# Optimization experiments

Hardware: AMD Instinct MI355X
Metric: run time of the kernel (lower is better)

Reference implementation:

```python
import jax, jax.numpy as jnp
import numpy as np
import math

NH = 12      # num attention heads
WIN = 128    # one-sided sliding window
NG = 32      # number of global (prefix) tokens
NEG = -1e9
LN_EPS = 1e-12


def _layernorm(x, g, b):
    mu = jnp.mean(x, axis=-1, keepdims=True)
    var = jnp.mean(jnp.square(x - mu), axis=-1, keepdims=True)
    return (x - mu) * jax.lax.rsqrt(var + LN_EPS) * g + b


def _longformer_self_attn(h, am, Wq, bq, Wk, bk, Wv, bv):
    B, S, D = h.shape
    Dh = D // NH
    w = WIN
    C = S // w  # number of chunks

    def proj(Wm, bm):
        return (h @ Wm + bm).reshape(B, S, NH, Dh).transpose(0, 2, 1, 3)

    q = proj(Wq, bq) * (1.0 / math.sqrt(Dh))  # [B,H,S,Dh]
    k = proj(Wk, bk)
    v = proj(Wv, bv)

    # ---- banded (sliding window) scores, chunked: each query chunk sees 3w keys ----
    kp = jnp.pad(k, ((0, 0), (0, 0), (w, w), (0, 0)))
    vp = jnp.pad(v, ((0, 0), (0, 0), (w, w), (0, 0)))
    idx = jnp.arange(C)[:, None] * w + jnp.arange(3 * w)[None, :]  # [C,3w]
    k3 = kp[:, :, idx]  # [B,H,C,3w,Dh]
    v3 = vp[:, :, idx]
    qc = q.reshape(B, NH, C, w, Dh)
    band = jnp.einsum('bhcqd,bhckd->bhcqk', qc, k3)  # [B,H,C,w,3w]

    qpos = (jnp.arange(C) * w)[:, None, None] + jnp.arange(w)[None, :, None]  # [C,w,1]
    kpos = (idx - w)[:, None, :]  # [C,1,3w] absolute key positions
    valid = (jnp.abs(kpos - qpos) <= w) & (kpos >= NG) & (kpos < S)  # band, exclude global keys

    amp = jnp.pad(am, ((0, 0), (w, w)))
    am3 = amp[:, idx]  # [B,C,3w] additive mask gathered per chunk
    band = band + am3[:, None, :, None, :]
    band = jnp.where(valid[None, None], band, NEG)
    band = band.reshape(B, NH, S, 3 * w)

    # ---- every token also attends to the NG global tokens ----
    gsc = jnp.einsum('bhsd,bhgd->bhsg', q, k[:, :, :NG]) + am[:, None, None, :NG]

    logits = jnp.concatenate([band, gsc], axis=-1)  # [B,H,S,3w+NG]
    probs = jax.nn.softmax(logits, axis=-1)
    pb = probs[..., :3 * w].reshape(B, NH, C, w, 3 * w)
    out = jnp.einsum('bhcqk,bhckd->bhcqd', pb, v3).reshape(B, NH, S, Dh)
    out = out + jnp.einsum('bhsg,bhgd->bhsd', probs[..., 3 * w:], v[:, :, :NG])

    # ---- global tokens attend to everything ----
    gl = jnp.einsum('bhgd,bhsd->bhgs', q[:, :, :NG], k) + am[:, None, None, :]
    outg = jnp.einsum('bhgs,bhsd->bhgd', jax.nn.softmax(gl, axis=-1), v)

    ctx = jnp.concatenate([outg, out[:, :, NG:]], axis=2)  # [B,H,S,Dh]
    return ctx.transpose(0, 2, 1, 3).reshape(B, S, D)


def setup_inputs() -> dict:
    key = jax.random.key(0)
    ks = jax.random.split(key, 8)
    B, S, D, F = 2, 4096, 768, 3072
    p = lambda k_, sh: jax.random.normal(k_, sh, jnp.float32) * 0.02
    return {
        'hidden_states': jax.random.normal(ks[0], (B, S, D), jnp.float32),
        'attention_mask': jnp.zeros((B, S), jnp.float32),
        'Wq': p(ks[1], (D, D)), 'bq': jnp.zeros((D,), jnp.float32),
        'Wk': p(ks[2], (D, D)), 'bk': jnp.zeros((D,), jnp.float32),
        'Wv': p(ks[3], (D, D)), 'bv': jnp.zeros((D,), jnp.float32),
        'Wo': p(ks[4], (D, D)), 'bo': jnp.zeros((D,), jnp.float32),
        'ln1_g': jnp.ones((D,), jnp.float32), 'ln1_b': jnp.zeros((D,), jnp.float32),
        'Wi': p(ks[5], (D, F)), 'bi': jnp.zeros((F,), jnp.float32),
        'Wo2': p(ks[6], (F, D)), 'bo2': jnp.zeros((D,), jnp.float32),
        'ln2_g': jnp.ones((D,), jnp.float32), 'ln2_b': jnp.zeros((D,), jnp.float32),
    }


def reference(hidden_states, attention_mask, Wq, bq, Wk, bk, Wv, bv, Wo, bo,
              ln1_g, ln1_b, Wi, bi, Wo2, bo2, ln2_g, ln2_b):
    ctx = _longformer_self_attn(hidden_states, attention_mask, Wq, bq, Wk, bk, Wv, bv)
    attn_out = _layernorm(ctx @ Wo + bo + hidden_states, ln1_g, ln1_b)
    inter = jax.nn.gelu(attn_out @ Wi + bi, approximate=False)
    layer_out = _layernorm(inter @ Wo2 + bo2 + attn_out, ln2_g, ln2_b)
    return layer_out
```

## Files before the change

### kernel.cpp

```cpp
#include <hip/hip_runtime.h>
#include <math.h>

#define NHEAD 12
#define DH 64
#define S_LEN 4096
#define B_SZ 2
#define D_MODEL 768
#define FF_DIM 3072
#define WINSZ 128
#define NGLB 32
#define NEGV -1e9f
#define NQC 6291456L

typedef __attribute__((ext_vector_type(8))) short bf16x8;
typedef __attribute__((ext_vector_type(4))) float floatx4;

__device__ __forceinline__ unsigned short f2bf(float x) {
    union { float f; unsigned u; } v; v.f = x;
    unsigned r = v.u + 0x7fffu + ((v.u >> 16) & 1u);
    return (unsigned short)(r >> 16);
}
__device__ __forceinline__ float bf2f(unsigned short x) {
    union { unsigned u; float f; } v; v.u = ((unsigned)x) << 16;
    return v.f;
}

__device__ __forceinline__ void async_copy16(const unsigned short* g, unsigned short* l) {
    __builtin_amdgcn_global_load_lds(
        (const __attribute__((address_space(1))) void*)g,
        (__attribute__((address_space(3))) void*)l, 16, 0, 0);
}

__global__ __launch_bounds__(256) void prep_k(
    const float* __restrict__ Wq, const float* __restrict__ Wk,
    const float* __restrict__ Wv, const float* __restrict__ Wo,
    const float* __restrict__ Wi, const float* __restrict__ Wo2,
    unsigned short* __restrict__ wqt, unsigned short* __restrict__ wkt,
    unsigned short* __restrict__ wvt, unsigned short* __restrict__ wot,
    unsigned short* __restrict__ wit, unsigned short* __restrict__ wo2t,
    const float* __restrict__ bq, const float* __restrict__ bk,
    const float* __restrict__ bv, float* __restrict__ bcat,
    const float* __restrict__ hid, unsigned short* __restrict__ hidb)
{
    __shared__ float tile[32][33];
    const int bid = blockIdx.x;
    const int tx = threadIdx.x, ty = threadIdx.y;

    if (bid < 6912) {
        const float* src; unsigned short* dst; int K, N, nx, local; float scale = 1.f;
        if (bid < 576)       { src = Wq;  dst = wqt;  K = 768;  N = 768;  nx = 24; local = bid;        scale = 0.125f; }
        else if (bid < 1152) { src = Wk;  dst = wkt;  K = 768;  N = 768;  nx = 24; local = bid - 576;  }
        else if (bid < 1728) { src = Wv;  dst = wvt;  K = 768;  N = 768;  nx = 24; local = bid - 1152; }
        else if (bid < 2304) { src = Wo;  dst = wot;  K = 768;  N = 768;  nx = 24; local = bid - 1728; }
        else if (bid < 4608) { src = Wi;  dst = wit;  K = 768;  N = 3072; nx = 96; local = bid - 2304; }
        else                 { src = Wo2; dst = wo2t; K = 3072; N = 768;  nx = 24; local = bid - 4608; }
        const int n0 = (local % nx) * 32, k0 = (local / nx) * 32;
#pragma unroll
        for (int i = 0; i < 4; ++i)
            tile[ty + 8 * i][tx] = src[(long)(k0 + ty + 8 * i) * N + n0 + tx];
        __syncthreads();
#pragma unroll
        for (int i = 0; i < 4; ++i)
            dst[(long)(n0 + ty + 8 * i) * K + k0 + tx] = f2bf(tile[tx][ty + 8 * i] * scale);
    } else if (bid < 6921) {
        const int t = ty * 32 + tx;
        const int i = (bid - 6912) * 256 + t;
        if (i < 768) bcat[i] = bq[i] * 0.125f;
        else if (i < 1536) bcat[i] = bk[i - 768];
        else if (i < 2304) bcat[i] = bv[i - 1536];
    } else {
        const int t = ty * 32 + tx;
        const long i = ((long)(bid - 6921) * 256 + t) * 4;
        float4 v = *(const float4*)(hid + i);
        ushort4 o;
        o.x = f2bf(v.x); o.y = f2bf(v.y); o.z = f2bf(v.z); o.w = f2bf(v.w);
        *(ushort4*)(hidb + i) = o;
    }
}

__global__ __launch_bounds__(256) void vt_k(
    const unsigned short* __restrict__ v, unsigned short* __restrict__ vt)
{
    const int bh = blockIdx.y;
    const int s0 = blockIdx.x * 32;
    const int w = threadIdx.x >> 6, lane = threadIdx.x & 63;
    const unsigned short* src = v + ((long)bh * S_LEN + s0 + w * 8) * DH + lane;
    unsigned short r[8];
#pragma unroll
    for (int j = 0; j < 8; ++j) r[j] = src[j * DH];
    unsigned short* dst = vt + ((long)bh * DH + lane) * S_LEN + s0 + w * 8;
    ushort4 lo, hi;
    lo.x = r[0]; lo.y = r[1]; lo.z = r[2]; lo.w = r[3];
    hi.x = r[4]; hi.y = r[5]; hi.z = r[6]; hi.w = r[7];
    *(ushort4*)dst = lo;
    *(ushort4*)(dst + 4) = hi;
}

template <int EPI>
__global__ __launch_bounds__(256) void gemm_bf(
    const unsigned short* __restrict__ A, const unsigned short* __restrict__ BT,
    const float* __restrict__ bias, void* __restrict__ out,
    int M, int N, int K, int nx)
{
    __shared__ unsigned short As[128 * 32];
    __shared__ unsigned short Bs[128 * 32];
    const int tid = threadIdx.x;
    const int wave = tid >> 6, lane = tid & 63;
    const int t8 = (blockIdx.x & 7) * (gridDim.x >> 3) + (blockIdx.x >> 3);
    const int m0 = (t8 / nx) * 128, n0 = (t8 % nx) * 128;
    const int wr = (wave >> 1) * 64, wc = (wave & 1) * 64;

    floatx4 acc[4][4];
#pragma unroll
    for (int i = 0; i < 4; ++i)
#pragma unroll
        for (int j = 0; j < 4; ++j) acc[i][j] = (floatx4){0.f, 0.f, 0.f, 0.f};

    const int srow = lane >> 2;
    const int schk = (((lane & 3) ^ (srow & 3))) * 8;
    const int r = lane & 15;
    const int q8 = ((lane >> 4) ^ (lane & 3)) * 8;

    for (int k0 = 0; k0 < K; k0 += 32) {
#pragma unroll
        for (int gi = 0; gi < 2; ++gi) {
            const int g = wave * 2 + gi;
            async_copy16(A + (long)(m0 + g * 16 + srow) * K + k0 + schk, &As[g * 512]);
            async_copy16(BT + (long)(n0 + g * 16 + srow) * K + k0 + schk, &Bs[g * 512]);
        }
        __syncthreads();

        bf16x8 af[4], bfr[4];
#pragma unroll
        for (int i = 0; i < 4; ++i) {
            af[i]  = *(const bf16x8*)&As[(wr + i * 16 + r) * 32 + q8];
            bfr[i] = *(const bf16x8*)&Bs[(wc + i * 16 + r) * 32 + q8];
        }
#pragma unroll
        for (int i = 0; i < 4; ++i)
#pragma unroll
            for (int j = 0; j < 4; ++j)
                acc[i][j] = __builtin_amdgcn_mfma_f32_16x16x32_bf16(
                    af[i], bfr[j], acc[i][j], 0, 0, 0);
        __syncthreads();
    }

    const int col_l = lane & 15, row_l = (lane >> 4) * 4;
#pragma unroll
    for (int i = 0; i < 4; ++i) {
#pragma unroll
        for (int j = 0; j < 4; ++j) {
            const int n = n0 + wc + j * 16 + col_l;
            const float bv = bias[n];
#pragma unroll
            for (int rg = 0; rg < 4; ++rg) {
                const int m = m0 + wr + i * 16 + row_l + rg;
                float v = acc[i][j][rg] + bv;
                if (EPI == 1) {
                    v = 0.5f * v * (1.f + erff(v * 0.70710678118654752f));
                    ((unsigned short*)out)[(long)m * N + n] = f2bf(v);
                } else {
                    const int bb = m >> 12, s = m & 4095;
                    const int part = n / 768;
                    const int nn = n - part * 768;
                    const int hh = nn >> 6, dh = nn & 63;
                    ((unsigned short*)out)[(long)part * NQC +
                        (((long)bb * NHEAD + hh) * S_LEN + s) * DH + dh] = f2bf(v);
                }
            }
        }
    }
}

__global__ __launch_bounds__(256) void gemm_sp(
    const unsigned short* __restrict__ A, const unsigned short* __restrict__ BT,
    float* __restrict__ p0, float* __restrict__ p1,
    int M, int N, int K2, int nx, int ntile)
{
    __shared__ unsigned short As[128 * 32];
    __shared__ unsigned short Bs[128 * 32];
    const int tid = threadIdx.x;
    const int wave = tid >> 6, lane = tid & 63;
    const int t8 = (blockIdx.x & 7) * (gridDim.x >> 3) + (blockIdx.x >> 3);
    const int slice = t8 >= ntile;
    const int tile = t8 - slice * ntile;
    const int m0 = (tile / nx) * 128, n0 = (tile % nx) * 128;
    const int kbeg = slice * K2, kend = kbeg + K2;
    float* P = slice ? p1 : p0;
    const int wr = (wave >> 1) * 64, wc = (wave & 1) * 64;

    floatx4 acc[4][4];
#pragma unroll
    for (int i = 0; i < 4; ++i)
#pragma unroll
        for (int j = 0; j < 4; ++j) acc[i][j] = (floatx4){0.f, 0.f, 0.f, 0.f};

    const int srow = lane >> 2;
    const int schk = (((lane & 3) ^ (srow & 3))) * 8;
    const int r = lane & 15;
    const int q8 = ((lane >> 4) ^ (lane & 3)) * 8;
    const long Kl = (long)K2 * 2;

    for (int k0 = kbeg; k0 < kend; k0 += 32) {
#pragma unroll
        for (int gi = 0; gi < 2; ++gi) {
            const int g = wave * 2 + gi;
            async_copy16(A + (long)(m0 + g * 16 + srow) * Kl + k0 + schk, &As[g * 512]);
            async_copy16(BT + (long)(n0 + g * 16 + srow) * Kl + k0 + schk, &Bs[g * 512]);
        }
        __syncthreads();

        bf16x8 af[4], bfr[4];
#pragma unroll
        for (int i = 0; i < 4; ++i) {
            af[i]  = *(const bf16x8*)&As[(wr + i * 16 + r) * 32 + q8];
            bfr[i] = *(const bf16x8*)&Bs[(wc + i * 16 + r) * 32 + q8];
        }
#pragma unroll
        for (int i = 0; i < 4; ++i)
#pragma unroll
            for (int j = 0; j < 4; ++j)
                acc[i][j] = __builtin_amdgcn_mfma_f32_16x16x32_bf16(
                    af[i], bfr[j], acc[i][j], 0, 0, 0);
        __syncthreads();
    }

    const int col_l = lane & 15, row_l = (lane >> 4) * 4;
#pragma unroll
    for (int i = 0; i < 4; ++i)
#pragma unroll
        for (int j = 0; j < 4; ++j) {
            const int n = n0 + wc + j * 16 + col_l;
#pragma unroll
            for (int rg = 0; rg < 4; ++rg) {
                const int m = m0 + wr + i * 16 + row_l + rg;
                P[(long)m * N + n] = acc[i][j][rg];
            }
        }
}

__global__ __launch_bounds__(256) void attn_k(
    const unsigned short* __restrict__ q, const unsigned short* __restrict__ k,
    const unsigned short* __restrict__ vt, const float* __restrict__ am,
    unsigned short* __restrict__ ctx)
{
    __shared__ __align__(16) unsigned char smem[28800];
    const int blk = blockIdx.x;
    const int tid = threadIdx.x;
    const int wave = tid >> 6, lane = tid & 63;
    const int ln15 = lane & 15, ln4 = lane >> 4;

    if (blk >= 24) {
        unsigned short* Ks = (unsigned short*)smem;
        unsigned short* Vs = Ks + 32 * 72;
        unsigned short* Ps = Vs + 64 * 40;

        const int bb = blk - 24;
        const int c = bb & 31;
        const int h = (bb >> 5) % NHEAD;
        const int b = bb / (32 * NHEAD);
        const long bh = (long)b * NHEAD + h;

        const unsigned short* kh  = k + bh * S_LEN * DH;
        const unsigned short* vth = vt + bh * (long)DH * S_LEN;
        const float* amb = am + (long)b * S_LEN;

        const int q0 = c * WINSZ + wave * 32;

        bf16x8 qf[2][2];
#pragma unroll
        for (int nt = 0; nt < 2; ++nt)
#pragma unroll
            for (int ks = 0; ks < 2; ++ks)
                qf[nt][ks] = *(const bf16x8*)(q + (bh * S_LEN + q0 + nt * 16 + ln15) * DH
                                              + ks * 32 + ln4 * 8);

        floatx4 o[4][2];
#pragma unroll
        for (int mt = 0; mt < 4; ++mt)
#pragma unroll
            for (int nt = 0; nt < 2; ++nt) o[mt][nt] = (floatx4){0.f, 0.f, 0.f, 0.f};
        float m_r[2] = {-1e30f, -1e30f}, l_r[2] = {0.f, 0.f};

        const int sk_key = tid >> 3, sk_ch = tid & 7;
        const int sv_dim = tid & 63, sv_ch = tid >> 6;
        const bf16x8 zero8 = {0, 0, 0, 0, 0, 0, 0, 0};

        for (int tile = 0; tile < 13; ++tile) {
            const bool glob = (tile == 12);
            const int kbase = glob ? 0 : (c * WINSZ - WINSZ + tile * 32);

            __syncthreads();
            {
                int kpos = kbase + sk_key;
                bf16x8 val = zero8;
                if ((unsigned)kpos < (unsigned)S_LEN)
                    val = *(const bf16x8*)(kh + (long)kpos * DH + sk_ch * 8);
                *(bf16x8*)(&Ks[sk_key * 72 + sk_ch * 8]) = val;
            }
            {
                int kc = kbase + sv_ch * 8;
                bf16x8 val = zero8;
                if (kc >= 0 && kc + 8 <= S_LEN)
                    val = *(const bf16x8*)(vth + (long)sv_dim * S_LEN + kc);
                *(bf16x8*)(&Vs[sv_dim * 40 + sv_ch * 8]) = val;
            }
            __syncthreads();

            bf16x8 ak[2][2];
#pragma unroll
            for (int mt = 0; mt < 2; ++mt)
#pragma unroll
                for (int ks = 0; ks < 2; ++ks)
                    ak[mt][ks] = *(const bf16x8*)(&Ks[(mt * 16 + ln15) * 72 + ks * 32 + ln4 * 8]);

            floatx4 s[2][2];
#pragma unroll
            for (int mt = 0; mt < 2; ++mt)
#pragma unroll
                for (int nt = 0; nt < 2; ++nt) {
                    floatx4 acc = (floatx4){0.f, 0.f, 0.f, 0.f};
                    acc = __builtin_amdgcn_mfma_f32_16x16x32_bf16(ak[mt][0], qf[nt][0], acc, 0, 0, 0);
                    acc = __builtin_amdgcn_mfma_f32_16x16x32_bf16(ak[mt][1], qf[nt][1], acc, 0, 0, 0);
                    s[mt][nt] = acc;
                }

#pragma unroll
            for (int mt = 0; mt < 2; ++mt) {
                const int kp0 = kbase + mt * 16 + ln4 * 4;
#pragma unroll
                for (int rg = 0; rg < 4; ++rg) {
                    const int kpos = kp0 + rg;
                    const bool kin = (unsigned)kpos < (unsigned)S_LEN;
                    const float amv = kin ? amb[kpos] : 0.f;
#pragma unroll
                    for (int nt = 0; nt < 2; ++nt) {
                        const int qpos = q0 + nt * 16 + ln15;
                        const int dlt = kpos > qpos ? kpos - qpos : qpos - kpos;
                        const bool valid = glob || (kpos >= NGLB && kin && dlt <= WINSZ);
                        s[mt][nt][rg] = valid ? s[mt][nt][rg] + amv : NEGV;
                    }
                }
            }

            float alpha[2];
#pragma unroll
            for (int nt = 0; nt < 2; ++nt) {
                float mx = s[0][nt][0];
#pragma unroll
                for (int rg = 1; rg < 4; ++rg) mx = fmaxf(mx, s[0][nt][rg]);
#pragma unroll
                for (int rg = 0; rg < 4; ++rg) mx = fmaxf(mx, s[1][nt][rg]);
                mx = fmaxf(mx, __shfl_xor(mx, 16));
                mx = fmaxf(mx, __shfl_xor(mx, 32));
                const float mn = fmaxf(m_r[nt], mx);
                alpha[nt] = __expf(m_r[nt] - mn);
                m_r[nt] = mn;
            }

#pragma unroll
            for (int nt = 0; nt < 2; ++nt) {
                float sum = 0.f;
#pragma unroll
                for (int mt = 0; mt < 2; ++mt) {
                    ushort4 pk;
#pragma unroll
                    for (int rg = 0; rg < 4; ++rg) {
                        const float p = __expf(s[mt][nt][rg] - m_r[nt]);
                        sum += p;
                        ((unsigned short*)&pk)[rg] = f2bf(p);
                    }
                    *(ushort4*)(&Ps[wave * 1280 + (nt * 16 + ln15) * 40 + mt * 16 + ln4 * 4]) = pk;
                }
                sum += __shfl_xor(sum, 16);
                sum += __shfl_xor(sum, 32);
                l_r[nt] = l_r[nt] * alpha[nt] + sum;
            }

#pragma unroll
            for (int mt = 0; mt < 4; ++mt)
#pragma unroll
                for (int nt = 0; nt < 2; ++nt)
#pragma unroll
                    for (int rg = 0; rg < 4; ++rg) o[mt][nt][rg] *= alpha[nt];

            bf16x8 av[4], bp[2];
#pragma unroll
            for (int mt = 0; mt < 4; ++mt)
                av[mt] = *(const bf16x8*)(&Vs[(mt * 16 + ln15) * 40 + ln4 * 8]);
#pragma unroll
            for (int nt = 0; nt < 2; ++nt)
                bp[nt] = *(const bf16x8*)(&Ps[wave * 1280 + (nt * 16 + ln15) * 40 + ln4 * 8]);
#pragma unroll
            for (int mt = 0; mt < 4; ++mt)
#pragma unroll
                for (int nt = 0; nt < 2; ++nt)
                    o[mt][nt] = __builtin_amdgcn_mfma_f32_16x16x32_bf16(
                        av[mt], bp[nt], o[mt][nt], 0, 0, 0);
        }

        if (q0 >= NGLB) {
            const float inv0 = 1.f / l_r[0], inv1 = 1.f / l_r[1];
#pragma unroll
            for (int nt = 0; nt < 2; ++nt) {
                const float inv = nt ? inv1 : inv0;
                const long row = (long)b * S_LEN + q0 + nt * 16 + ln15;
#pragma unroll
                for (int mt = 0; mt < 4; ++mt) {
                    ushort4 ov;
#pragma unroll
                    for (int rg = 0; rg < 4; ++rg)
                        ((unsigned short*)&ov)[rg] = f2bf(o[mt][nt][rg] * inv);
                    *(ushort4*)(ctx + row * D_MODEL + h * DH + mt * 16 + ln4 * 4) = ov;
                }
            }
        }
    } else {
        unsigned short* Psg = (unsigned short*)smem;
        float* Om   = (float*)(smem + 18432);
        float* mW   = (float*)(smem + 27648);
        float* lW   = (float*)(smem + 28160);
        float* lTot = (float*)(smem + 28672);

        const int bh = blk;
        const int b = bh / NHEAD, h = bh % NHEAD;

        const unsigned short* kh  = k + (long)bh * S_LEN * DH;
        const unsigned short* vth = vt + (long)bh * DH * S_LEN;
        const float* amb = am + (long)b * S_LEN;

        bf16x8 qf[2][2];
#pragma unroll
        for (int nt = 0; nt < 2; ++nt)
#pragma unroll
            for (int ks = 0; ks < 2; ++ks)
                qf[nt][ks] = *(const bf16x8*)(q + ((long)bh * S_LEN + nt * 16 + ln15) * DH
                                              + ks * 32 + ln4 * 8);

        floatx4 o[4][2];
#pragma unroll
        for (int mt = 0; mt < 4; ++mt)
#pragma unroll
            for (int nt = 0; nt < 2; ++nt) o[mt][nt] = (floatx4){0.f, 0.f, 0.f, 0.f};
        float m_r[2] = {-1e30f, -1e30f}, l_r[2] = {0.f, 0.f};

        for (int it = 0; it < 16; ++it) {
            const int kbase = it * 256 + wave * 64;

            bf16x8 ak[4][2];
#pragma unroll
            for (int mt = 0; mt < 4; ++mt)
#pragma unroll
                for (int ks = 0; ks < 2; ++ks)
                    ak[mt][ks] = *(const bf16x8*)(kh + (long)(kbase + mt * 16 + ln15) * DH
                                                  + ks * 32 + ln4 * 8);

            floatx4 s[4][2];
#pragma unroll
            for (int mt = 0; mt < 4; ++mt)
#pragma unroll
                for (int nt = 0; nt < 2; ++nt) {
                    floatx4 acc = (floatx4){0.f, 0.f, 0.f, 0.f};
                    acc = __builtin_amdgcn_mfma_f32_16x16x32_bf16(ak[mt][0], qf[nt][0], acc, 0, 0, 0);
                    acc = __builtin_amdgcn_mfma_f32_16x16x32_bf16(ak[mt][1], qf[nt][1], acc, 0, 0, 0);
                    s[mt][nt] = acc;
                }

#pragma unroll
            for (int mt = 0; mt < 4; ++mt) {
                const int kp0 = kbase + mt * 16 + ln4 * 4;
#pragma unroll
                for (int rg = 0; rg < 4; ++rg) {
                    const float amv = amb[kp0 + rg];
#pragma unroll
                    for (int nt = 0; nt < 2; ++nt) s[mt][nt][rg] += amv;
                }
            }

            float alpha[2];
#pragma unroll
            for (int nt = 0; nt < 2; ++nt) {
                float mx = s[0][nt][0];
#pragma unroll
                for (int mt = 0; mt < 4; ++mt)
#pragma unroll
                    for (int rg = 0; rg < 4; ++rg) mx = fmaxf(mx, s[mt][nt][rg]);
                mx = fmaxf(mx, __shfl_xor(mx, 16));
                mx = fmaxf(mx, __shfl_xor(mx, 32));
                const float mn = fmaxf(m_r[nt], mx);
                alpha[nt] = __expf(m_r[nt] - mn);
                m_r[nt] = mn;
            }

#pragma unroll
            for (int nt = 0; nt < 2; ++nt) {
                float sum = 0.f;
#pragma unroll
                for (int mt = 0; mt < 4; ++mt) {
                    ushort4 pk;
#pragma unroll
                    for (int rg = 0; rg < 4; ++rg) {
                        const float p = __expf(s[mt][nt][rg] - m_r[nt]);
                        sum += p;
                        ((unsigned short*)&pk)[rg] = f2bf(p);
                    }
                    *(ushort4*)(&Psg[wave * 2304 + (nt * 16 + ln15) * 72 + mt * 16 + ln4 * 4]) = pk;
                }
                sum += __shfl_xor(sum, 16);
                sum += __shfl_xor(sum, 32);
                l_r[nt] = l_r[nt] * alpha[nt] + sum;
            }

#pragma unroll
            for (int mt = 0; mt < 4; ++mt)
#pragma unroll
                for (int nt = 0; nt < 2; ++nt)
#pragma unroll
                    for (int rg = 0; rg < 4; ++rg) o[mt][nt][rg] *= alpha[nt];

            bf16x8 av[4][2], bp[2][2];
#pragma unroll
            for (int mt = 0; mt < 4; ++mt)
#pragma unroll
                for (int ks = 0; ks < 2; ++ks)
                    av[mt][ks] = *(const bf16x8*)(vth + (long)(mt * 16 + ln15) * S_LEN
                                                  + kbase + ks * 32 + ln4 * 8);
#pragma unroll
            for (int nt = 0; nt < 2; ++nt)
#pragma unroll
                for (int ks = 0; ks < 2; ++ks)
                    bp[nt][ks] = *(const bf16x8*)(&Psg[wave * 2304 + (nt * 16 + ln15) * 72
                                                  + ks * 32 + ln4 * 8]);
#pragma unroll
            for (int mt = 0; mt < 4; ++mt)
#pragma unroll
                for (int nt = 0; nt < 2; ++nt) {
                    o[mt][nt] = __builtin_amdgcn_mfma_f32_16x16x32_bf16(
                        av[mt][0], bp[nt][0], o[mt][nt], 0, 0, 0);
                    o[mt][nt] = __builtin_amdgcn_mfma_f32_16x16x32_bf16(
                        av[mt][1], bp[nt][1], o[mt][nt], 0, 0, 0);
                }
        }

        if (ln4 == 0) {
#pragma unroll
            for (int nt = 0; nt < 2; ++nt) {
                mW[wave * 32 + nt * 16 + ln15] = m_r[nt];
                lW[wave * 32 + nt * 16 + ln15] = l_r[nt];
            }
        }
        for (int i = tid; i < 64 * 36; i += 256) Om[i] = 0.f;
        __syncthreads();

        float f[2];
#pragma unroll
        for (int nt = 0; nt < 2; ++nt) {
            const int qq = nt * 16 + ln15;
            float mt_ = mW[qq];
#pragma unroll
            for (int w = 1; w < 4; ++w) mt_ = fmaxf(mt_, mW[w * 32 + qq]);
            float lt = 0.f;
#pragma unroll
            for (int w = 0; w < 4; ++w) lt += __expf(mW[w * 32 + qq] - mt_) * lW[w * 32 + qq];
            f[nt] = __expf(m_r[nt] - mt_);
            if (wave == 0 && ln4 == 0) lTot[qq] = lt;
        }
#pragma unroll
        for (int mt = 0; mt < 4; ++mt)
#pragma unroll
            for (int nt = 0; nt < 2; ++nt)
#pragma unroll
                for (int rg = 0; rg < 4; ++rg) o[mt][nt][rg] *= f[nt];

        for (int wv = 0; wv < 4; ++wv) {
            if (wave == wv) {
#pragma unroll
                for (int mt = 0; mt < 4; ++mt)
#pragma unroll
                    for (int nt = 0; nt < 2; ++nt)
#pragma unroll
                        for (int rg = 0; rg < 4; ++rg)
                            Om[(mt * 16 + ln4 * 4 + rg) * 36 + nt * 16 + ln15] += o[mt][nt][rg];
            }
            __syncthreads();
        }

        const int qq = tid >> 3, d0 = (tid & 7) * 8;
        const float inv = 1.f / lTot[qq];
        ushort4 ov0, ov1;
#pragma unroll
        for (int i = 0; i < 4; ++i)
            ((unsigned short*)&ov0)[i] = f2bf(Om[(d0 + i) * 36 + qq] * inv);
#pragma unroll
        for (int i = 0; i < 4; ++i)
            ((unsigned short*)&ov1)[i] = f2bf(Om[(d0 + 4 + i) * 36 + qq] * inv);
        unsigned short* dst = ctx + ((long)b * S_LEN + qq) * D_MODEL + h * DH + d0;
        *(ushort4*)dst = ov0;
        *(ushort4*)(dst + 4) = ov1;
    }
}

__global__ __launch_bounds__(256) void ln2p_k(
    const float* __restrict__ p0, const float* __restrict__ p1,
    const float* __restrict__ bias, const float* __restrict__ resid,
    float* __restrict__ out, unsigned short* __restrict__ out_bf,
    const float* __restrict__ gw, const float* __restrict__ bw)
{
    __shared__ float red[8];
    const long base = (long)blockIdx.x * D_MODEL;
    const int t = threadIdx.x;
    const int wv = t >> 6, lane = t & 63;
    float v0 = p0[base + t]       + p1[base + t]       + bias[t]       + resid[base + t];
    float v1 = p0[base + t + 256] + p1[base + t + 256] + bias[t + 256] + resid[base + t + 256];
    float v2 = p0[base + t + 512] + p1[base + t + 512] + bias[t + 512] + resid[base + t + 512];

    float s = v0 + v1 + v2;
#pragma unroll
    for (int off = 32; off; off >>= 1) s += __shfl_xor(s, off);
    if (lane == 0) red[wv] = s;
    __syncthreads();
    const float mu = (red[0] + red[1] + red[2] + red[3]) * (1.f / 768.f);

    const float d0 = v0 - mu, d1 = v1 - mu, d2 = v2 - mu;
    float s2 = d0 * d0 + d1 * d1 + d2 * d2;
#pragma unroll
    for (int off = 32; off; off >>= 1) s2 += __shfl_xor(s2, off);
    if (lane == 0) red[4 + wv] = s2;
    __syncthreads();
    const float var = (red[4] + red[5] + red[6] + red[7]) * (1.f / 768.f);
    const float rs = rsqrtf(var + 1e-12f);

    const float y0 = d0 * rs * gw[t] + bw[t];
    const float y1 = d1 * rs * gw[t + 256] + bw[t + 256];
    const float y2 = d2 * rs * gw[t + 512] + bw[t + 512];
    if (out) {
        float* y = out + base;
        y[t] = y0; y[t + 256] = y1; y[t + 512] = y2;
    }
    if (out_bf) {
        unsigned short* yb = out_bf + base;
        yb[t] = f2bf(y0); yb[t + 256] = f2bf(y1); yb[t + 512] = f2bf(y2);
    }
}

extern "C" void kernel_launch(void* const* d_in, const int* in_sizes, int n_in,
                              void* d_out, int out_size, void* d_ws, size_t ws_size,
                              hipStream_t stream)
{
    const float* hid  = (const float*)d_in[0];
    const float* am   = (const float*)d_in[1];
    const float* Wq   = (const float*)d_in[2];
    const float* bq   = (const float*)d_in[3];
    const float* Wk   = (const float*)d_in[4];
    const float* bk   = (const float*)d_in[5];
    const float* Wv   = (const float*)d_in[6];
    const float* bv   = (const float*)d_in[7];
    const float* Wo   = (const float*)d_in[8];
    const float* bo   = (const float*)d_in[9];
    const float* ln1g = (const float*)d_in[10];
    const float* ln1b = (const float*)d_in[11];
    const float* Wi   = (const float*)d_in[12];
    const float* bi   = (const float*)d_in[13];
    const float* Wo2  = (const float*)d_in[14];
    const float* bo2  = (const float*)d_in[15];
    const float* ln2g = (const float*)d_in[16];
    const float* ln2b = (const float*)d_in[17];

    const long M  = (long)B_SZ * S_LEN;
    const long NQ = NQC;

    unsigned short* W16 = (unsigned short*)d_ws;
    unsigned short* qb   = W16;
    unsigned short* kb   = W16 + NQ;
    unsigned short* vb   = W16 + 2 * NQ;
    unsigned short* vtb  = W16 + 3 * NQ;
    unsigned short* ctxb = W16 + 4 * NQ;
    unsigned short* hidb = W16 + 5 * NQ;
    unsigned short* wqt  = W16 + 6 * NQ;
    unsigned short* wkt  = wqt + 589824;
    unsigned short* wvt  = wkt + 589824;
    unsigned short* wot  = wvt + 589824;
    unsigned short* wit  = wot + 589824;
    unsigned short* wo2t = wit + 2359296;
    float* tmp   = (float*)(W16 + 44826624);
    float* partB1 = (float*)(W16 + 57409536);
    float* bcat  = (float*)(W16 + 69992448);
    float* partA0 = (float*)W16;
    float* partA1 = (float*)(W16 + 2 * NQ);
    unsigned short* interb = W16;
    unsigned short* attnb  = hidb;
    float* partB0 = (float*)(W16 + 4 * NQ);
    (void)ws_size; (void)in_sizes; (void)n_in; (void)out_size;

    prep_k<<<dim3(13065), dim3(32, 8), 0, stream>>>(
        Wq, Wk, Wv, Wo, Wi, Wo2, wqt, wkt, wvt, wot, wit, wo2t,
        bq, bk, bv, bcat, hid, hidb);

    dim3 blk(256);

    gemm_bf<2><<<dim3(1152), blk, 0, stream>>>(hidb, wqt, bcat, qb,
                                               M, 2304, 768, 18);

    vt_k<<<dim3(128, 24), blk, 0, stream>>>(vb, vtb);

    attn_k<<<dim3(792), blk, 0, stream>>>(qb, kb, vtb, am, ctxb);

    gemm_sp<<<dim3(768), blk, 0, stream>>>(ctxb, wot, partA0, partA1,
                                           M, 768, 384, 6, 384);
    ln2p_k<<<dim3(M), blk, 0, stream>>>(partA0, partA1, bo, hid,
                                        tmp, attnb, ln1g, ln1b);

    gemm_bf<1><<<dim3(1536), blk, 0, stream>>>(attnb, wit, bi, interb,
                                               M, 3072, 768, 24);

    gemm_sp<<<dim3(768), blk, 0, stream>>>(interb, wo2t, partB0, partB1,
                                           M, 768, 1536, 6, 384);
    ln2p_k<<<dim3(M), blk, 0, stream>>>(partB0, partB1, bo2, tmp,
                                        (float*)d_out, nullptr, ln2g, ln2b);
}
```

Baseline: 422.0 us.

## Double-buffer LDS tiles in bf16 GEMM kernels to overlap loads with MFMA

Both GEMM kernels (gemm_bf and gemm_sp) now keep two LDS buffers for the A and B tiles. The async copy of the next K-slice is issued before the MFMAs on the current slice, which leaves one barrier per iteration instead of two and hides global-load latency behind compute. It also raises the MFMA section's wave priority with s_setprio and adds a sched_barrier. LDS use doubles to 32KB per block, which may reduce occupancy. Correctness depends on the async copies having landed by the single __syncthreads at the end of each iteration.

```diff
diff --git a/kernel.cpp b/kernel.cpp
--- a/kernel.cpp
+++ b/kernel.cpp
@@ -102,8 +102,8 @@
     const float* __restrict__ bias, void* __restrict__ out,
     int M, int N, int K, int nx)
 {
-    __shared__ unsigned short As[128 * 32];
-    __shared__ unsigned short Bs[128 * 32];
+    __shared__ unsigned short As[2][128 * 32];
+    __shared__ unsigned short Bs[2][128 * 32];
     const int tid = threadIdx.x;
     const int wave = tid >> 6, lane = tid & 63;
     const int t8 = (blockIdx.x & 7) * (gridDim.x >> 3) + (blockIdx.x >> 3);
@@ -121,27 +121,44 @@
     const int r = lane & 15;
     const int q8 = ((lane >> 4) ^ (lane & 3)) * 8;
 
-    for (int k0 = 0; k0 < K; k0 += 32) {
-#pragma unroll
-        for (int gi = 0; gi < 2; ++gi) {
-            const int g = wave * 2 + gi;
-            async_copy16(A + (long)(m0 + g * 16 + srow) * K + k0 + schk, &As[g * 512]);
-            async_copy16(BT + (long)(n0 + g * 16 + srow) * K + k0 + schk, &Bs[g * 512]);
-        }
-        __syncthreads();
+    const int NT = K >> 5;
+    const unsigned short* aSrc0 = A  + (long)(m0 + wave * 32 + srow) * K + schk;
+    const unsigned short* aSrc1 = A  + (long)(m0 + wave * 32 + 16 + srow) * K + schk;
+    const unsigned short* bSrc0 = BT + (long)(n0 + wave * 32 + srow) * K + schk;
+    const unsigned short* bSrc1 = BT + (long)(n0 + wave * 32 + 16 + srow) * K + schk;
+    const int g0 = wave * 1024, g1 = wave * 1024 + 512;
+
+    async_copy16(aSrc0, &As[0][g0]);
+    async_copy16(bSrc0, &Bs[0][g0]);
+    async_copy16(aSrc1, &As[0][g1]);
+    async_copy16(bSrc1, &Bs[0][g1]);
+    __syncthreads();
+
+    for (int t = 0; t < NT; ++t) {
+        const int cur = t & 1;
+        if (t + 1 < NT) {
+            const int k0 = (t + 1) << 5;
+            async_copy16(aSrc0 + k0, &As[cur ^ 1][g0]);
+            async_copy16(bSrc0 + k0, &Bs[cur ^ 1][g0]);
+            async_copy16(aSrc1 + k0, &As[cur ^ 1][g1]);
+            async_copy16(bSrc1 + k0, &Bs[cur ^ 1][g1]);
+        }
+        __builtin_amdgcn_sched_barrier(0);
 
         bf16x8 af[4], bfr[4];
 #pragma unroll
         for (int i = 0; i < 4; ++i) {
-            af[i]  = *(const bf16x8*)&As[(wr + i * 16 + r) * 32 + q8];
-            bfr[i] = *(const bf16x8*)&Bs[(wc + i * 16 + r) * 32 + q8];
-        }
+            af[i]  = *(const bf16x8*)&As[cur][(wr + i * 16 + r) * 32 + q8];
+            bfr[i] = *(const bf16x8*)&Bs[cur][(wc + i * 16 + r) * 32 + q8];
+        }
+        __builtin_amdgcn_s_setprio(1);
 #pragma unroll
         for (int i = 0; i < 4; ++i)
 #pragma unroll
             for (int j = 0; j < 4; ++j)
                 acc[i][j] = __builtin_amdgcn_mfma_f32_16x16x32_bf16(
                     af[i], bfr[j], acc[i][j], 0, 0, 0);
+        __builtin_amdgcn_s_setprio(0);
         __syncthreads();
     }
 
@@ -177,15 +194,15 @@
     float* __restrict__ p0, float* __restrict__ p1,
     int M, int N, int K2, int nx, int ntile)
 {
-    __shared__ unsigned short As[128 * 32];
-    __shared__ unsigned short Bs[128 * 32];
+    __shared__ unsigned short As[2][128 * 32];
+    __shared__ unsigned short Bs[2][128 * 32];
     const int tid = threadIdx.x;
     const int wave = tid >> 6, lane = tid & 63;
     const int t8 = (blockIdx.x & 7) * (gridDim.x >> 3) + (blockIdx.x >> 3);
     const int slice = t8 >= ntile;
     const int tile = t8 - slice * ntile;
     const int m0 = (tile / nx) * 128, n0 = (tile % nx) * 128;
-    const int kbeg = slice * K2, kend = kbeg + K2;
+    const int kbeg = slice * K2;
     float* P = slice ? p1 : p0;
     const int wr = (wave >> 1) * 64, wc = (wave & 1) * 64;
 
@@ -201,27 +218,44 @@
     const int q8 = ((lane >> 4) ^ (lane & 3)) * 8;
     const long Kl = (long)K2 * 2;
 
-    for (int k0 = kbeg; k0 < kend; k0 += 32) {
-#pragma unroll
-        for (int gi = 0; gi < 2; ++gi) {
-            const int g = wave * 2 + gi;
-            async_copy16(A + (long)(m0 + g * 16 + srow) * Kl + k0 + schk, &As[g * 512]);
-            async_copy16(BT + (long)(n0 + g * 16 + srow) * Kl + k0 + schk, &Bs[g * 512]);
-        }
-        __syncthreads();
+    const int NT = K2 >> 5;
+    const unsigned short* aSrc0 = A  + (long)(m0 + wave * 32 + srow) * Kl + kbeg + schk;
+    const unsigned short* aSrc1 = A  + (long)(m0 + wave * 32 + 16 + srow) * Kl + kbeg + schk;
+    const unsigned short* bSrc0 = BT + (long)(n0 + wave * 32 + srow) * Kl + kbeg + schk;
+    const unsigned short* bSrc1 = BT + (long)(n0 + wave * 32 + 16 + srow) * Kl + kbeg + schk;
+    const int g0 = wave * 1024, g1 = wave * 1024 + 512;
+
+    async_copy16(aSrc0, &As[0][g0]);
+    async_copy16(bSrc0, &Bs[0][g0]);
+    async_copy16(aSrc1, &As[0][g1]);
+    async_copy16(bSrc1, &Bs[0][g1]);
+    __syncthreads();
+
+    for (int t = 0; t < NT; ++t) {
+        const int cur = t & 1;
+        if (t + 1 < NT) {
+            const int k0 = (t + 1) << 5;
+            async_copy16(aSrc0 + k0, &As[cur ^ 1][g0]);
+            async_copy16(bSrc0 + k0, &Bs[cur ^ 1][g0]);
+            async_copy16(aSrc1 + k0, &As[cur ^ 1][g1]);
+            async_copy16(bSrc1 + k0, &Bs[cur ^ 1][g1]);
+        }
+        __builtin_amdgcn_sched_barrier(0);
 
         bf16x8 af[4], bfr[4];
 #pragma unroll
         for (int i = 0; i < 4; ++i) {
-            af[i]  = *(const bf16x8*)&As[(wr + i * 16 + r) * 32 + q8];
-            bfr[i] = *(const bf16x8*)&Bs[(wc + i * 16 + r) * 32 + q8];
-        }
+            af[i]  = *(const bf16x8*)&As[cur][(wr + i * 16 + r) * 32 + q8];
+            bfr[i] = *(const bf16x8*)&Bs[cur][(wc + i * 16 + r) * 32 + q8];
+        }
+        __builtin_amdgcn_s_setprio(1);
 #pragma unroll
         for (int i = 0; i < 4; ++i)
 #pragma unroll
             for (int j = 0; j < 4; ++j)
                 acc[i][j] = __builtin_amdgcn_mfma_f32_16x16x32_bf16(
                     af[i], bfr[j], acc[i][j], 0, 0, 0);
+        __builtin_amdgcn_s_setprio(0);
         __syncthreads();
     }
 
```

Result: faster. 411.9 us (-2.4%).
